# Optimization experiments

Hardware: AMD Instinct MI355X
Metric: run time of the kernel (lower is better)

Reference implementation:

```python
import jax, jax.numpy as jnp
import numpy as np

N = 100_000   # nodes
E = 1_600_000 # directed edges
G = 2048      # graphs in batch
NF = 78       # input node features
DIM = 32      # GIN hidden dim
L = 5         # num GIN layers
OUT = 128     # output_dim
BN_EPS = 1e-5


def setup_inputs() -> dict:
    key = jax.random.key(0)
    ks = jax.random.split(key, 8)
    s = 0.1
    return {
        "x": jax.random.normal(ks[0], (N, NF), jnp.float32),
        "edge_index": jax.random.randint(ks[1], (2, E), 0, N, jnp.int32),
        "batch": jnp.sort(jax.random.randint(ks[2], (N,), 0, G, jnp.int32)),
        "W1_0": (jax.random.normal(ks[3], (NF, DIM), jnp.float32) * s),
        "W1_rest": (jax.random.normal(ks[4], (L - 1, DIM, DIM), jnp.float32) * s),
        "b1": jnp.zeros((L, DIM), jnp.float32),
        "W2": (jax.random.normal(ks[5], (L, DIM, DIM), jnp.float32) * s),
        "b2": jnp.zeros((L, DIM), jnp.float32),
        "gamma": jnp.ones((L, DIM), jnp.float32),
        "beta": jnp.zeros((L, DIM), jnp.float32),
        "Wfc": (jax.random.normal(ks[6], (DIM, OUT), jnp.float32) * s),
        "bfc": jnp.zeros((OUT,), jnp.float32),
    }


def reference(x, edge_index, batch, W1_0, W1_rest, b1, W2, b2, gamma, beta, Wfc, bfc):
    src, dst = edge_index[0], edge_index[1]
    h = x
    for i in range(L):
        # GINConv (eps=0): h_i' = MLP(h_i + sum_{j->i} h_j)
        agg = jax.ops.segment_sum(h[src], dst, num_segments=N)  # [N, d]
        h = h + agg
        W1 = W1_0 if i == 0 else W1_rest[i - 1]
        h = jnp.maximum(h @ W1 + b1[i], 0.0) @ W2[i] + b2[i]
        # ReLU then BatchNorm1d (training mode: batch stats, biased var)
        h = jnp.maximum(h, 0.0)
        mu = h.mean(axis=0)
        var = h.var(axis=0)
        h = gamma[i] * (h - mu) * jax.lax.rsqrt(var + BN_EPS) + beta[i]
    pooled = jax.ops.segment_sum(h, batch, num_segments=G)  # global_add_pool [G, DIM]
    return jnp.maximum(pooled @ Wfc + bfc, 0.0)  # dropout is identity (eval)
```

## Files before the change

kernel.cpp:

```cpp
#include <hip/hip_runtime.h>
#include <hip/hip_fp16.h>

#define N_NODES 100000
#define N_EDGES 1600000
#define N_GRAPHS 2048
#define NFEAT 78
#define DIM 32
#define NLAYERS 5
#define OUTD 128
#define BN_EPS 1e-5f
#define NPB 32
#define NBUK 391
#define BNODES 256
#define STRIDE 4608
#define EPB 4096
#define NBLK ((N_EDGES + EPB - 1) / EPB)
#define NSLOTS2 ((N_NODES / NPB + 63) / 64)

__device__ __forceinline__ float2 up2(unsigned u) {
    __half2 h = *reinterpret_cast<__half2*>(&u);
    return __half22float2(h);
}
__device__ __forceinline__ unsigned pk2(float a, float b) {
    __half2 h = __floats2half2_rn(a, b);
    return *reinterpret_cast<unsigned*>(&h);
}

__global__ __launch_bounds__(256) void prep_kernel(
    const int* __restrict__ ei, int* __restrict__ bcnt, int* __restrict__ bdata,
    const float* __restrict__ x, const float* __restrict__ W1_0,
    unsigned short* __restrict__ y)
{
    __shared__ int cur[NBUK];
    __shared__ int gbl[NBUK];
    __shared__ float Wl[NFEAT * DIM];
    int tid = threadIdx.x;

    if (blockIdx.x < NBLK) {
        int base = blockIdx.x * EPB;
        for (int i = tid; i < NBUK; i += 256) cur[i] = 0;
        __syncthreads();

        int ew[16], eb[16];
        const int4* s4 = (const int4*)ei;
        const int4* d4 = (const int4*)(ei + N_EDGES);
#pragma unroll
        for (int c = 0; c < 4; ++c) {
            int eidx = base + c * 1024 + tid * 4;
            if (eidx < N_EDGES) {
                int4 sv = s4[eidx >> 2];
                int4 dv = d4[eidx >> 2];
                ew[c*4+0] = sv.x | ((dv.x & 255) << 17); eb[c*4+0] = dv.x >> 8;
                ew[c*4+1] = sv.y | ((dv.y & 255) << 17); eb[c*4+1] = dv.y >> 8;
                ew[c*4+2] = sv.z | ((dv.z & 255) << 17); eb[c*4+2] = dv.z >> 8;
                ew[c*4+3] = sv.w | ((dv.w & 255) << 17); eb[c*4+3] = dv.w >> 8;
            } else {
                eb[c*4+0] = eb[c*4+1] = eb[c*4+2] = eb[c*4+3] = -1;
                ew[c*4+0] = ew[c*4+1] = ew[c*4+2] = ew[c*4+3] = 0;
            }
        }
        int slot[16];
#pragma unroll
        for (int k = 0; k < 16; ++k)
            slot[k] = (eb[k] >= 0) ? atomicAdd(&cur[eb[k]], 1) : 0;
        __syncthreads();
        for (int b = tid; b < NBUK; b += 256) {
            int c = cur[b];
            gbl[b] = (c > 0) ? atomicAdd(&bcnt[b], c) : 0;
        }
        __syncthreads();
#pragma unroll
        for (int k = 0; k < 16; ++k) {
            int b = eb[k];
            if (b >= 0) {
                int pos = gbl[b] + slot[k];
                if (pos < STRIDE) bdata[b * STRIDE + pos] = ew[k];
            }
        }
    } else {
        for (int i = tid; i < NFEAT * DIM; i += 256) Wl[i] = W1_0[i];
        __syncthreads();
        int t = (blockIdx.x - NBLK) * 256 + tid;
        int row = t >> 3;
        int c0 = (t & 7) * 4;
        float a0 = 0.f, a1 = 0.f, a2 = 0.f, a3 = 0.f;
        const float* hr = x + (long)row * NFEAT;
        for (int k = 0; k < NFEAT; ++k) {
            float xv = hr[k];
            a0 = fmaf(xv, Wl[k * DIM + c0 + 0], a0);
            a1 = fmaf(xv, Wl[k * DIM + c0 + 1], a1);
            a2 = fmaf(xv, Wl[k * DIM + c0 + 2], a2);
            a3 = fmaf(xv, Wl[k * DIM + c0 + 3], a3);
        }
        ((uint2*)y)[(long)row * 8 + (t & 7)] = make_uint2(pk2(a0, a1), pk2(a2, a3));
    }
}

__global__ __launch_bounds__(512) void bscan_kernel(
    const int* __restrict__ bcnt, int* __restrict__ bbase)
{
    __shared__ int sd[512];
    int t = threadIdx.x;
    int v = (t < NBUK) ? min(bcnt[t], STRIDE) : 0;
    sd[t] = v; __syncthreads();
    for (int off = 1; off < 512; off <<= 1) {
        int a = (t >= off) ? sd[t - off] : 0;
        __syncthreads();
        sd[t] += a;
        __syncthreads();
    }
    if (t < NBUK) bbase[t + 1] = sd[t];
    if (t == 0) bbase[0] = 0;
}

__global__ __launch_bounds__(256) void cfill2_kernel(
    const int* __restrict__ bcnt, const int* __restrict__ bbase,
    const int* __restrict__ bdata, int* __restrict__ edge_src,
    int* __restrict__ offs)
{
    __shared__ int sorted[STRIDE];
    __shared__ int cnt[BNODES], off[BNODES], cur[BNODES];
    int b = blockIdx.x, tid = threadIdx.x;
    int n = min(bcnt[b], STRIDE);
    int gb = bbase[b];
    const int* slab = bdata + (long)b * STRIDE;

    if (tid < BNODES) cnt[tid] = 0;
    __syncthreads();
    for (int i = tid; i < n; i += 256)
        atomicAdd(&cnt[slab[i] >> 17], 1);
    __syncthreads();
    int t = tid;
    if (t < BNODES) off[t] = cnt[t];
    __syncthreads();
    for (int o = 1; o < BNODES; o <<= 1) {
        int a = (t >= o && t < BNODES) ? off[t - o] : 0;
        __syncthreads();
        if (t < BNODES) off[t] += a;
        __syncthreads();
    }
    if (t < BNODES) {
        int excl = off[t] - cnt[t];
        off[t] = excl;
        cur[t] = excl;
        int node = b * BNODES + t;
        if (node <= N_NODES) offs[node] = gb + excl;
    }
    __syncthreads();
    for (int i = tid; i < n; i += 256) {
        int w = slab[i];
        int pos = atomicAdd(&cur[w >> 17], 1);
        sorted[pos] = w & 0x1FFFF;
    }
    __syncthreads();
    for (int i = tid; i < n; i += 256)
        edge_src[gb + i] = sorted[i];
}

template<bool MM>
__global__ __launch_bounds__(256) void layer_kernel(
    const int* __restrict__ offs, const int* __restrict__ edge_src,
    const unsigned short* __restrict__ zin, const float* __restrict__ W1p,
    const float* __restrict__ cvec, const float* __restrict__ b1v,
    const float* __restrict__ W2, const float* __restrict__ b2v,
    unsigned short* __restrict__ zout, float* __restrict__ partial)
{
    __shared__ float W1l[DIM * DIM];
    __shared__ float W2l[DIM * DIM];
    __shared__ float zs[NPB][36];
    __shared__ float srow[NPB][36];
    __shared__ float b1l[DIM], b2l[DIM], cl[DIM];
    __shared__ float psum[DIM], psq[DIM];

    int tid = threadIdx.x;
    if (MM) for (int i = tid; i < DIM * DIM; i += 256) W1l[i] = W1p[i];
    for (int i = tid; i < DIM * DIM; i += 256) W2l[i] = W2[i];
    if (tid < DIM) {
        b1l[tid] = b1v[tid]; b2l[tid] = b2v[tid];
        cl[tid] = MM ? cvec[tid] : 0.f;
        psum[tid] = 0.f; psq[tid] = 0.f;
    }
    __syncthreads();

    int ln = tid >> 3, p = tid & 7;
    int c0 = p * 4;
    long node = (long)blockIdx.x * NPB + ln;
    int beg = offs[node], end = offs[node + 1];
    int deg = end - beg;
    const uint2* zb = (const uint2*)zin;

    uint2 sv = zb[node * 8 + p];
    float2 t01 = up2(sv.x), t23 = up2(sv.y);
    float a0 = t01.x, a1 = t01.y, a2 = t23.x, a3 = t23.y;
    int e = beg;
    for (; e + 8 <= end; e += 8) {
        uint2 v0 = zb[(long)edge_src[e + 0] * 8 + p];
        uint2 v1 = zb[(long)edge_src[e + 1] * 8 + p];
        uint2 v2 = zb[(long)edge_src[e + 2] * 8 + p];
        uint2 v3 = zb[(long)edge_src[e + 3] * 8 + p];
        uint2 v4 = zb[(long)edge_src[e + 4] * 8 + p];
        uint2 v5 = zb[(long)edge_src[e + 5] * 8 + p];
        uint2 v6 = zb[(long)edge_src[e + 6] * 8 + p];
        uint2 v7 = zb[(long)edge_src[e + 7] * 8 + p];
        float2 f;
        f = up2(v0.x); a0 += f.x; a1 += f.y;  f = up2(v0.y); a2 += f.x; a3 += f.y;
        f = up2(v1.x); a0 += f.x; a1 += f.y;  f = up2(v1.y); a2 += f.x; a3 += f.y;
        f = up2(v2.x); a0 += f.x; a1 += f.y;  f = up2(v2.y); a2 += f.x; a3 += f.y;
        f = up2(v3.x); a0 += f.x; a1 += f.y;  f = up2(v3.y); a2 += f.x; a3 += f.y;
        f = up2(v4.x); a0 += f.x; a1 += f.y;  f = up2(v4.y); a2 += f.x; a3 += f.y;
        f = up2(v5.x); a0 += f.x; a1 += f.y;  f = up2(v5.y); a2 += f.x; a3 += f.y;
        f = up2(v6.x); a0 += f.x; a1 += f.y;  f = up2(v6.y); a2 += f.x; a3 += f.y;
        f = up2(v7.x); a0 += f.x; a1 += f.y;  f = up2(v7.y); a2 += f.x; a3 += f.y;
    }
    for (; e < end; ++e) {
        uint2 v = zb[(long)edge_src[e] * 8 + p];
        float2 f;
        f = up2(v.x); a0 += f.x; a1 += f.y;
        f = up2(v.y); a2 += f.x; a3 += f.y;
    }
    *(float4*)&zs[ln][c0] = make_float4(a0, a1, a2, a3);

    float sv4[4];
    if (MM) {
        sv4[0] = sv4[1] = sv4[2] = sv4[3] = 0.f;
#pragma unroll
        for (int k = 0; k < DIM; ++k) {
            float zk = zs[ln][k];
            sv4[0] = fmaf(zk, W1l[k * DIM + c0 + 0], sv4[0]);
            sv4[1] = fmaf(zk, W1l[k * DIM + c0 + 1], sv4[1]);
            sv4[2] = fmaf(zk, W1l[k * DIM + c0 + 2], sv4[2]);
            sv4[3] = fmaf(zk, W1l[k * DIM + c0 + 3], sv4[3]);
        }
        float dp1 = (float)(deg + 1);
#pragma unroll
        for (int j = 0; j < 4; ++j)
            sv4[j] = fmaf(dp1, cl[c0 + j], sv4[j]) + b1l[c0 + j];
    } else {
        sv4[0] = a0 + b1l[c0 + 0]; sv4[1] = a1 + b1l[c0 + 1];
        sv4[2] = a2 + b1l[c0 + 2]; sv4[3] = a3 + b1l[c0 + 3];
    }
    float4 srw = make_float4(fmaxf(sv4[0], 0.f), fmaxf(sv4[1], 0.f),
                             fmaxf(sv4[2], 0.f), fmaxf(sv4[3], 0.f));
    *(float4*)&srow[ln][c0] = srw;

    float zv[4] = { b2l[c0 + 0], b2l[c0 + 1], b2l[c0 + 2], b2l[c0 + 3] };
#pragma unroll
    for (int k = 0; k < DIM; ++k) {
        float sk = srow[ln][k];
        zv[0] = fmaf(sk, W2l[k * DIM + c0 + 0], zv[0]);
        zv[1] = fmaf(sk, W2l[k * DIM + c0 + 1], zv[1]);
        zv[2] = fmaf(sk, W2l[k * DIM + c0 + 2], zv[2]);
        zv[3] = fmaf(sk, W2l[k * DIM + c0 + 3], zv[3]);
    }
#pragma unroll
    for (int j = 0; j < 4; ++j) zv[j] = fmaxf(zv[j], 0.f);
    ((uint2*)zout)[node * 8 + p] = make_uint2(pk2(zv[0], zv[1]), pk2(zv[2], zv[3]));

    float sq[4];
#pragma unroll
    for (int j = 0; j < 4; ++j) sq[j] = zv[j] * zv[j];
#pragma unroll
    for (int off = 8; off < 64; off <<= 1) {
#pragma unroll
        for (int j = 0; j < 4; ++j) {
            zv[j] += __shfl_xor(zv[j], off, 64);
            sq[j] += __shfl_xor(sq[j], off, 64);
        }
    }
    if ((tid & 63) < 8) {
#pragma unroll
        for (int j = 0; j < 4; ++j) {
            atomicAdd(&psum[c0 + j], zv[j]);
            atomicAdd(&psq[c0 + j], sq[j]);
        }
    }
    __syncthreads();
    if (tid < 2 * DIM) {
        float v = (tid < DIM) ? psum[tid] : psq[tid - DIM];
        atomicAdd(&partial[(long)(blockIdx.x >> 6) * 2 * DIM + tid], v);
    }
}

__global__ __launch_bounds__(256) void finalize_kernel(
    const float* __restrict__ partial,
    const float* __restrict__ gamma, const float* __restrict__ beta,
    float* __restrict__ ss, const float* W1next,
    float* __restrict__ W1p, float* __restrict__ cvec)
{
    __shared__ float red[256];
    __shared__ float sscl[DIM], sshl[DIM];
    int t = threadIdx.x;
    int c = t & 63;
    int chunk = t >> 6;
    float a = 0.f;
    for (int p = chunk; p < NSLOTS2; p += 4) a += partial[(long)p * 64 + c];
    red[t] = a; __syncthreads();
    if (t < 64) red[t] = red[t] + red[t + 64] + red[t + 128] + red[t + 192];
    __syncthreads();
    if (t < DIM) {
        const float invN = 1.0f / (float)N_NODES;
        float S = red[t], Q = red[t + DIM];
        float mu = S * invN;
        float var = Q * invN - mu * mu;
        float scale = gamma[t] * rsqrtf(var + BN_EPS);
        float shift = beta[t] - mu * scale;
        ss[t] = scale; ss[DIM + t] = shift;
        sscl[t] = scale; sshl[t] = shift;
    }
    __syncthreads();
    if (W1next) {
        for (int i = t; i < DIM * DIM; i += 256)
            W1p[i] = sscl[i >> 5] * W1next[i];
        if (t < DIM) {
            float cv = 0.f;
            for (int k = 0; k < DIM; ++k)
                cv += sshl[k] * W1next[k * DIM + t];
            cvec[t] = cv;
        }
    }
}

__global__ __launch_bounds__(256) void pool_kernel(
    const unsigned short* __restrict__ z, const int* __restrict__ batch,
    const float* __restrict__ ss, float* __restrict__ pooled)
{
    __shared__ float acc[32][32];
    __shared__ int slot[32];
    __shared__ int segg[32];
    __shared__ int nsegS;
    __shared__ float scl[DIM], shl[DIM];
    int tid = threadIdx.x;
    for (int i = tid; i < 1024; i += 256) ((float*)acc)[i] = 0.f;
    if (tid < DIM) { scl[tid] = ss[tid]; shl[tid] = ss[DIM + tid]; }
    int nodeBase = blockIdx.x * 32;
    if (tid < 32) {
        int nd = nodeBase + tid;
        int gv = batch[nd];
        int flag = (tid == 0) ? 1 : (gv != batch[nd - 1]);
        unsigned long long m = __ballot(flag);
        int s = __popcll(m & ((2ull << tid) - 1ull)) - 1;
        slot[tid] = s;
        if (flag) segg[s] = gv;
        if (tid == 0) nsegS = __popcll(m);
    }
    __syncthreads();

    int ln = tid >> 3;
    int p = tid & 7;
    long node = nodeBase + ln;
    uint2 u = ((const uint2*)z)[node * 8 + p];
    int c = p * 4;
    float2 f01 = up2(u.x), f23 = up2(u.y);
    float vx = fmaf(f01.x, scl[c+0], shl[c+0]);
    float vy = fmaf(f01.y, scl[c+1], shl[c+1]);
    float vz = fmaf(f23.x, scl[c+2], shl[c+2]);
    float vw = fmaf(f23.y, scl[c+3], shl[c+3]);
    int s = slot[ln];
    atomicAdd(&acc[s][c+0], vx);
    atomicAdd(&acc[s][c+1], vy);
    atomicAdd(&acc[s][c+2], vz);
    atomicAdd(&acc[s][c+3], vw);
    __syncthreads();

    int total = nsegS * 32;
    for (int i = tid; i < total; i += 256) {
        int r = i >> 5, dd = i & 31;
        float val = acc[r][dd];
        if (val != 0.f) atomicAdd(&pooled[(long)segg[r] * DIM + dd], val);
    }
}

__global__ __launch_bounds__(256) void fc_kernel(
    const float* __restrict__ pooled, const float* __restrict__ Wfc,
    const float* __restrict__ bfc, float* __restrict__ out)
{
    __shared__ float Wl[DIM * OUTD];
    for (int i = threadIdx.x; i < DIM * OUTD; i += 256) Wl[i] = Wfc[i];
    __syncthreads();
    int t = blockIdx.x * 256 + threadIdx.x;
    if (t >= N_GRAPHS * OUTD) return;
    int g = t >> 7;
    int o = t & (OUTD - 1);
    float acc = bfc[o];
    const float* pr = pooled + (long)g * DIM;
#pragma unroll
    for (int k = 0; k < DIM; ++k) acc += pr[k] * Wl[k * OUTD + o];
    out[t] = fmaxf(acc, 0.f);
}

extern "C" void kernel_launch(void* const* d_in, const int* in_sizes, int n_in,
                              void* d_out, int out_size, void* d_ws, size_t ws_size,
                              hipStream_t stream) {
    const float* x      = (const float*)d_in[0];
    const int*   ei     = (const int*)  d_in[1];
    const int*   batch  = (const int*)  d_in[2];
    const float* W1_0   = (const float*)d_in[3];
    const float* W1_rest= (const float*)d_in[4];
    const float* b1     = (const float*)d_in[5];
    const float* W2     = (const float*)d_in[6];
    const float* b2     = (const float*)d_in[7];
    const float* gamma  = (const float*)d_in[8];
    const float* beta   = (const float*)d_in[9];
    const float* Wfc    = (const float*)d_in[10];
    const float* bfc    = (const float*)d_in[11];
    float* out = (float*)d_out;

    int* wsi = (int*)d_ws;
    const size_t nf = (size_t)N_NODES * DIM;
    const size_t BD = (size_t)NBUK * STRIDE;
    int*   bdata  = wsi;
    unsigned short* zfpA = (unsigned short*)(wsi + BD);
    unsigned short* zfpB = zfpA + nf;
    int*   edge_src = (int*)(zfpB + nf);
    int*   offs   = edge_src + N_EDGES;
    int*   bcnt   = offs + (N_NODES + 1);
    int*   bbase  = bcnt + NBUK;
    float* pooled = (float*)(bbase + NBUK + 1);
    float* partial= pooled + (size_t)N_GRAPHS * DIM;
    float* ss     = partial + (size_t)NLAYERS * NSLOTS2 * 2 * DIM;
    float* W1p    = ss + NLAYERS * 2 * DIM;
    float* cvec   = W1p + NLAYERS * DIM * DIM;

    hipMemsetAsync(pooled, 0,
        ((size_t)N_GRAPHS * DIM + (size_t)NLAYERS * NSLOTS2 * 2 * DIM) *
        sizeof(float), stream);
    hipMemsetAsync(bcnt, 0, (size_t)NBUK * sizeof(int), stream);

    const int grpBlocks = (N_NODES * 8) / 256;

    prep_kernel<<<NBLK + grpBlocks, 256, 0, stream>>>(
        ei, bcnt, bdata, x, W1_0, zfpA);
    bscan_kernel<<<1, 512, 0, stream>>>(bcnt, bbase);
    cfill2_kernel<<<NBUK, 256, 0, stream>>>(bcnt, bbase, bdata, edge_src, offs);

    layer_kernel<false><<<N_NODES / NPB, 256, 0, stream>>>(
        offs, edge_src, zfpA, nullptr, nullptr,
        b1, W2, b2, zfpB, partial);
    finalize_kernel<<<1, 256, 0, stream>>>(
        partial, gamma, beta, ss,
        W1_rest, W1p + DIM * DIM, cvec + DIM);

    const unsigned short* zi = zfpB;
    unsigned short* zo = zfpA;
    for (int i = 1; i < NLAYERS; ++i) {
        layer_kernel<true><<<N_NODES / NPB, 256, 0, stream>>>(
            offs, edge_src, zi,
            W1p + (size_t)i * DIM * DIM, cvec + (size_t)i * DIM,
            b1 + i * DIM, W2 + (size_t)i * DIM * DIM, b2 + i * DIM,
            zo, partial + (size_t)i * NSLOTS2 * 2 * DIM);
        const float* W1next = (i + 1 < NLAYERS) ? (W1_rest + (size_t)i * DIM * DIM)
                                                : nullptr;
        finalize_kernel<<<1, 256, 0, stream>>>(
            partial + (size_t)i * NSLOTS2 * 2 * DIM,
            gamma + i * DIM, beta + i * DIM, ss + i * 2 * DIM,
            W1next, W1p + (size_t)(i + 1) * DIM * DIM,
            cvec + (size_t)(i + 1) * DIM);
        const unsigned short* tmp = zi; zi = zo; zo = (unsigned short*)tmp;
    }

    pool_kernel<<<N_NODES / 32, 256, 0, stream>>>(
        zi, batch, ss + (NLAYERS - 1) * 2 * DIM, pooled);
    fc_kernel<<<(N_GRAPHS * OUTD) / 256, 256, 0, stream>>>(pooled, Wfc, bfc, out);
}
```

Baseline: 301.4 us.

## Fuse BN finalize into layer and fc kernels; process two nodes per thread

Removes the single-block finalize kernel launches between layers. Each layer block now reduces the previous layer's partial BN statistics itself and folds scale and shift into W1. The final BN is applied algebraically in fc_kernel using per-graph node counts gathered by pool_kernel. Each layer block now handles 64 nodes, with each thread interleaving the gathers of two nodes to raise memory-level parallelism. The cost is redundant statistic reduction in every block and higher register use.

```diff
diff --git a/kernel.cpp b/kernel.cpp
--- a/kernel.cpp
+++ b/kernel.cpp
@@ -9,13 +9,13 @@
 #define NLAYERS 5
 #define OUTD 128
 #define BN_EPS 1e-5f
-#define NPB 32
 #define NBUK 391
 #define BNODES 256
 #define STRIDE 4608
 #define EPB 4096
 #define NBLK ((N_EDGES + EPB - 1) / EPB)
-#define NSLOTS2 ((N_NODES / NPB + 63) / 64)
+#define NLB ((N_NODES + 63) / 64)
+#define NSLOTS3 ((NLB + 63) / 64)
 
 __device__ __forceinline__ float2 up2(unsigned u) {
     __half2 h = *reinterpret_cast<__half2*>(&u);
@@ -160,117 +160,200 @@
 template<bool MM>
 __global__ __launch_bounds__(256) void layer_kernel(
     const int* __restrict__ offs, const int* __restrict__ edge_src,
-    const unsigned short* __restrict__ zin, const float* __restrict__ W1p,
-    const float* __restrict__ cvec, const float* __restrict__ b1v,
+    const unsigned short* __restrict__ zin,
+    const float* __restrict__ W1g,
+    const float* __restrict__ partial_prev,
+    const float* __restrict__ gprev, const float* __restrict__ bprev,
+    const float* __restrict__ b1v,
     const float* __restrict__ W2, const float* __restrict__ b2v,
     unsigned short* __restrict__ zout, float* __restrict__ partial)
 {
     __shared__ float W1l[DIM * DIM];
     __shared__ float W2l[DIM * DIM];
-    __shared__ float zs[NPB][36];
-    __shared__ float srow[NPB][36];
+    __shared__ float zs[64][36];
     __shared__ float b1l[DIM], b2l[DIM], cl[DIM];
+    __shared__ float sscl[DIM], sshl[DIM];
     __shared__ float psum[DIM], psq[DIM];
 
     int tid = threadIdx.x;
-    if (MM) for (int i = tid; i < DIM * DIM; i += 256) W1l[i] = W1p[i];
+    float* red = &zs[0][0];
+
     for (int i = tid; i < DIM * DIM; i += 256) W2l[i] = W2[i];
     if (tid < DIM) {
         b1l[tid] = b1v[tid]; b2l[tid] = b2v[tid];
-        cl[tid] = MM ? cvec[tid] : 0.f;
         psum[tid] = 0.f; psq[tid] = 0.f;
+    }
+    if (MM) {
+        int c = tid & 63, chunk = tid >> 6;
+        float a = 0.f;
+        for (int p = chunk; p < NSLOTS3; p += 4) a += partial_prev[p * 64 + c];
+        red[tid] = a;
+        __syncthreads();
+        if (tid < 64) red[tid] = red[tid] + red[tid+64] + red[tid+128] + red[tid+192];
+        __syncthreads();
+        if (tid < DIM) {
+            const float invN = 1.0f / (float)N_NODES;
+            float S = red[tid], Q = red[tid + DIM];
+            float mu = S * invN;
+            float var = Q * invN - mu * mu;
+            float sc = gprev[tid] * rsqrtf(var + BN_EPS);
+            sscl[tid] = sc;
+            sshl[tid] = bprev[tid] - mu * sc;
+        }
+        __syncthreads();
+        for (int i = tid; i < DIM * DIM; i += 256) W1l[i] = sscl[i >> 5] * W1g[i];
+        if (tid < DIM) {
+            float cv = 0.f;
+            for (int k = 0; k < DIM; ++k) cv = fmaf(sshl[k], W1g[k * DIM + tid], cv);
+            cl[tid] = cv;
+        }
     }
     __syncthreads();
 
     int ln = tid >> 3, p = tid & 7;
     int c0 = p * 4;
-    long node = (long)blockIdx.x * NPB + ln;
-    int beg = offs[node], end = offs[node + 1];
-    int deg = end - beg;
+    int nb = blockIdx.x * 64;
+    int nA = nb + ln;
+    int nB = nb + 32 + ln;
+    bool vB = nB < N_NODES;
+    int begA = offs[nA], endA = offs[nA + 1];
+    int begB = 0, endB = 0;
+    if (vB) { begB = offs[nB]; endB = offs[nB + 1]; }
+    int degA = endA - begA, degB = endB - begB;
     const uint2* zb = (const uint2*)zin;
 
-    uint2 sv = zb[node * 8 + p];
-    float2 t01 = up2(sv.x), t23 = up2(sv.y);
-    float a0 = t01.x, a1 = t01.y, a2 = t23.x, a3 = t23.y;
-    int e = beg;
-    for (; e + 8 <= end; e += 8) {
-        uint2 v0 = zb[(long)edge_src[e + 0] * 8 + p];
-        uint2 v1 = zb[(long)edge_src[e + 1] * 8 + p];
-        uint2 v2 = zb[(long)edge_src[e + 2] * 8 + p];
-        uint2 v3 = zb[(long)edge_src[e + 3] * 8 + p];
-        uint2 v4 = zb[(long)edge_src[e + 4] * 8 + p];
-        uint2 v5 = zb[(long)edge_src[e + 5] * 8 + p];
-        uint2 v6 = zb[(long)edge_src[e + 6] * 8 + p];
-        uint2 v7 = zb[(long)edge_src[e + 7] * 8 + p];
-        float2 f;
+    uint2 svA = zb[(long)nA * 8 + p];
+    float2 f;
+    f = up2(svA.x); float a0 = f.x, a1 = f.y;
+    f = up2(svA.y); float a2 = f.x, a3 = f.y;
+    float g0 = 0.f, g1 = 0.f, g2 = 0.f, g3 = 0.f;
+    if (vB) {
+        uint2 svB = zb[(long)nB * 8 + p];
+        f = up2(svB.x); g0 = f.x; g1 = f.y;
+        f = up2(svB.y); g2 = f.x; g3 = f.y;
+    }
+    int eA = begA, eB = begB;
+    for (; eA + 4 <= endA && eB + 4 <= endB; eA += 4, eB += 4) {
+        int sA0 = edge_src[eA+0], sA1 = edge_src[eA+1];
+        int sA2 = edge_src[eA+2], sA3 = edge_src[eA+3];
+        int sB0 = edge_src[eB+0], sB1 = edge_src[eB+1];
+        int sB2 = edge_src[eB+2], sB3 = edge_src[eB+3];
+        uint2 vA0 = zb[(long)sA0*8+p], vA1 = zb[(long)sA1*8+p];
+        uint2 vA2 = zb[(long)sA2*8+p], vA3 = zb[(long)sA3*8+p];
+        uint2 vB0 = zb[(long)sB0*8+p], vB1 = zb[(long)sB1*8+p];
+        uint2 vB2 = zb[(long)sB2*8+p], vB3 = zb[(long)sB3*8+p];
+        f = up2(vA0.x); a0 += f.x; a1 += f.y;  f = up2(vA0.y); a2 += f.x; a3 += f.y;
+        f = up2(vA1.x); a0 += f.x; a1 += f.y;  f = up2(vA1.y); a2 += f.x; a3 += f.y;
+        f = up2(vA2.x); a0 += f.x; a1 += f.y;  f = up2(vA2.y); a2 += f.x; a3 += f.y;
+        f = up2(vA3.x); a0 += f.x; a1 += f.y;  f = up2(vA3.y); a2 += f.x; a3 += f.y;
+        f = up2(vB0.x); g0 += f.x; g1 += f.y;  f = up2(vB0.y); g2 += f.x; g3 += f.y;
+        f = up2(vB1.x); g0 += f.x; g1 += f.y;  f = up2(vB1.y); g2 += f.x; g3 += f.y;
+        f = up2(vB2.x); g0 += f.x; g1 += f.y;  f = up2(vB2.y); g2 += f.x; g3 += f.y;
+        f = up2(vB3.x); g0 += f.x; g1 += f.y;  f = up2(vB3.y); g2 += f.x; g3 += f.y;
+    }
+    for (; eA + 4 <= endA; eA += 4) {
+        int s0 = edge_src[eA+0], s1 = edge_src[eA+1];
+        int s2 = edge_src[eA+2], s3 = edge_src[eA+3];
+        uint2 v0 = zb[(long)s0*8+p], v1 = zb[(long)s1*8+p];
+        uint2 v2 = zb[(long)s2*8+p], v3 = zb[(long)s3*8+p];
         f = up2(v0.x); a0 += f.x; a1 += f.y;  f = up2(v0.y); a2 += f.x; a3 += f.y;
         f = up2(v1.x); a0 += f.x; a1 += f.y;  f = up2(v1.y); a2 += f.x; a3 += f.y;
         f = up2(v2.x); a0 += f.x; a1 += f.y;  f = up2(v2.y); a2 += f.x; a3 += f.y;
         f = up2(v3.x); a0 += f.x; a1 += f.y;  f = up2(v3.y); a2 += f.x; a3 += f.y;
-        f = up2(v4.x); a0 += f.x; a1 += f.y;  f = up2(v4.y); a2 += f.x; a3 += f.y;
-        f = up2(v5.x); a0 += f.x; a1 += f.y;  f = up2(v5.y); a2 += f.x; a3 += f.y;
-        f = up2(v6.x); a0 += f.x; a1 += f.y;  f = up2(v6.y); a2 += f.x; a3 += f.y;
-        f = up2(v7.x); a0 += f.x; a1 += f.y;  f = up2(v7.y); a2 += f.x; a3 += f.y;
-    }
-    for (; e < end; ++e) {
-        uint2 v = zb[(long)edge_src[e] * 8 + p];
-        float2 f;
+    }
+    for (; eA < endA; ++eA) {
+        uint2 v = zb[(long)edge_src[eA]*8+p];
         f = up2(v.x); a0 += f.x; a1 += f.y;
         f = up2(v.y); a2 += f.x; a3 += f.y;
     }
-    *(float4*)&zs[ln][c0] = make_float4(a0, a1, a2, a3);
-
-    float sv4[4];
+    for (; eB + 4 <= endB; eB += 4) {
+        int s0 = edge_src[eB+0], s1 = edge_src[eB+1];
+        int s2 = edge_src[eB+2], s3 = edge_src[eB+3];
+        uint2 v0 = zb[(long)s0*8+p], v1 = zb[(long)s1*8+p];
+        uint2 v2 = zb[(long)s2*8+p], v3 = zb[(long)s3*8+p];
+        f = up2(v0.x); g0 += f.x; g1 += f.y;  f = up2(v0.y); g2 += f.x; g3 += f.y;
+        f = up2(v1.x); g0 += f.x; g1 += f.y;  f = up2(v1.y); g2 += f.x; g3 += f.y;
+        f = up2(v2.x); g0 += f.x; g1 += f.y;  f = up2(v2.y); g2 += f.x; g3 += f.y;
+        f = up2(v3.x); g0 += f.x; g1 += f.y;  f = up2(v3.y); g2 += f.x; g3 += f.y;
+    }
+    for (; eB < endB; ++eB) {
+        uint2 v = zb[(long)edge_src[eB]*8+p];
+        f = up2(v.x); g0 += f.x; g1 += f.y;
+        f = up2(v.y); g2 += f.x; g3 += f.y;
+    }
+    *(float4*)&zs[ln][c0]      = make_float4(a0, a1, a2, a3);
+    *(float4*)&zs[ln + 32][c0] = make_float4(g0, g1, g2, g3);
+
+    float tA[4], tB[4];
     if (MM) {
-        sv4[0] = sv4[1] = sv4[2] = sv4[3] = 0.f;
+        tA[0]=tA[1]=tA[2]=tA[3]=0.f; tB[0]=tB[1]=tB[2]=tB[3]=0.f;
 #pragma unroll
         for (int k = 0; k < DIM; ++k) {
+            float w0 = W1l[k * DIM + c0 + 0], w1 = W1l[k * DIM + c0 + 1];
+            float w2 = W1l[k * DIM + c0 + 2], w3 = W1l[k * DIM + c0 + 3];
             float zk = zs[ln][k];
-            sv4[0] = fmaf(zk, W1l[k * DIM + c0 + 0], sv4[0]);
-            sv4[1] = fmaf(zk, W1l[k * DIM + c0 + 1], sv4[1]);
-            sv4[2] = fmaf(zk, W1l[k * DIM + c0 + 2], sv4[2]);
-            sv4[3] = fmaf(zk, W1l[k * DIM + c0 + 3], sv4[3]);
-        }
-        float dp1 = (float)(deg + 1);
-#pragma unroll
-        for (int j = 0; j < 4; ++j)
-            sv4[j] = fmaf(dp1, cl[c0 + j], sv4[j]) + b1l[c0 + j];
+            tA[0] = fmaf(zk, w0, tA[0]); tA[1] = fmaf(zk, w1, tA[1]);
+            tA[2] = fmaf(zk, w2, tA[2]); tA[3] = fmaf(zk, w3, tA[3]);
+            float wk = zs[ln + 32][k];
+            tB[0] = fmaf(wk, w0, tB[0]); tB[1] = fmaf(wk, w1, tB[1]);
+            tB[2] = fmaf(wk, w2, tB[2]); tB[3] = fmaf(wk, w3, tB[3]);
+        }
+        float dA = (float)(degA + 1), dB = (float)(degB + 1);
+#pragma unroll
+        for (int j = 0; j < 4; ++j) {
+            tA[j] = fmaxf(fmaf(dA, cl[c0 + j], tA[j]) + b1l[c0 + j], 0.f);
+            tB[j] = fmaxf(fmaf(dB, cl[c0 + j], tB[j]) + b1l[c0 + j], 0.f);
+        }
     } else {
-        sv4[0] = a0 + b1l[c0 + 0]; sv4[1] = a1 + b1l[c0 + 1];
-        sv4[2] = a2 + b1l[c0 + 2]; sv4[3] = a3 + b1l[c0 + 3];
-    }
-    float4 srw = make_float4(fmaxf(sv4[0], 0.f), fmaxf(sv4[1], 0.f),
-                             fmaxf(sv4[2], 0.f), fmaxf(sv4[3], 0.f));
-    *(float4*)&srow[ln][c0] = srw;
-
-    float zv[4] = { b2l[c0 + 0], b2l[c0 + 1], b2l[c0 + 2], b2l[c0 + 3] };
+        tA[0] = fmaxf(a0 + b1l[c0 + 0], 0.f); tA[1] = fmaxf(a1 + b1l[c0 + 1], 0.f);
+        tA[2] = fmaxf(a2 + b1l[c0 + 2], 0.f); tA[3] = fmaxf(a3 + b1l[c0 + 3], 0.f);
+        tB[0] = fmaxf(g0 + b1l[c0 + 0], 0.f); tB[1] = fmaxf(g1 + b1l[c0 + 1], 0.f);
+        tB[2] = fmaxf(g2 + b1l[c0 + 2], 0.f); tB[3] = fmaxf(g3 + b1l[c0 + 3], 0.f);
+    }
+    *(float4*)&zs[ln][c0]      = make_float4(tA[0], tA[1], tA[2], tA[3]);
+    *(float4*)&zs[ln + 32][c0] = make_float4(tB[0], tB[1], tB[2], tB[3]);
+
+    float zA[4] = { b2l[c0+0], b2l[c0+1], b2l[c0+2], b2l[c0+3] };
+    float zB[4] = { b2l[c0+0], b2l[c0+1], b2l[c0+2], b2l[c0+3] };
 #pragma unroll
     for (int k = 0; k < DIM; ++k) {
-        float sk = srow[ln][k];
-        zv[0] = fmaf(sk, W2l[k * DIM + c0 + 0], zv[0]);
-        zv[1] = fmaf(sk, W2l[k * DIM + c0 + 1], zv[1]);
-        zv[2] = fmaf(sk, W2l[k * DIM + c0 + 2], zv[2]);
-        zv[3] = fmaf(sk, W2l[k * DIM + c0 + 3], zv[3]);
-    }
-#pragma unroll
-    for (int j = 0; j < 4; ++j) zv[j] = fmaxf(zv[j], 0.f);
-    ((uint2*)zout)[node * 8 + p] = make_uint2(pk2(zv[0], zv[1]), pk2(zv[2], zv[3]));
-
-    float sq[4];
-#pragma unroll
-    for (int j = 0; j < 4; ++j) sq[j] = zv[j] * zv[j];
+        float w0 = W2l[k * DIM + c0 + 0], w1 = W2l[k * DIM + c0 + 1];
+        float w2 = W2l[k * DIM + c0 + 2], w3 = W2l[k * DIM + c0 + 3];
+        float sk = zs[ln][k];
+        zA[0] = fmaf(sk, w0, zA[0]); zA[1] = fmaf(sk, w1, zA[1]);
+        zA[2] = fmaf(sk, w2, zA[2]); zA[3] = fmaf(sk, w3, zA[3]);
+        float rk = zs[ln + 32][k];
+        zB[0] = fmaf(rk, w0, zB[0]); zB[1] = fmaf(rk, w1, zB[1]);
+        zB[2] = fmaf(rk, w2, zB[2]); zB[3] = fmaf(rk, w3, zB[3]);
+    }
+#pragma unroll
+    for (int j = 0; j < 4; ++j) {
+        zA[j] = fmaxf(zA[j], 0.f);
+        zB[j] = fmaxf(zB[j], 0.f);
+    }
+    ((uint2*)zout)[(long)nA * 8 + p] = make_uint2(pk2(zA[0], zA[1]), pk2(zA[2], zA[3]));
+    if (vB)
+        ((uint2*)zout)[(long)nB * 8 + p] = make_uint2(pk2(zB[0], zB[1]), pk2(zB[2], zB[3]));
+    else { zB[0] = zB[1] = zB[2] = zB[3] = 0.f; }
+
+    float sv[4], sq[4];
+#pragma unroll
+    for (int j = 0; j < 4; ++j) {
+        sv[j] = zA[j] + zB[j];
+        sq[j] = zA[j]*zA[j] + zB[j]*zB[j];
+    }
 #pragma unroll
     for (int off = 8; off < 64; off <<= 1) {
 #pragma unroll
         for (int j = 0; j < 4; ++j) {
-            zv[j] += __shfl_xor(zv[j], off, 64);
+            sv[j] += __shfl_xor(sv[j], off, 64);
             sq[j] += __shfl_xor(sq[j], off, 64);
         }
     }
     if ((tid & 63) < 8) {
 #pragma unroll
         for (int j = 0; j < 4; ++j) {
-            atomicAdd(&psum[c0 + j], zv[j]);
+            atomicAdd(&psum[c0 + j], sv[j]);
             atomicAdd(&psq[c0 + j], sq[j]);
         }
     }
@@ -281,57 +364,18 @@
     }
 }
 
-__global__ __launch_bounds__(256) void finalize_kernel(
-    const float* __restrict__ partial,
-    const float* __restrict__ gamma, const float* __restrict__ beta,
-    float* __restrict__ ss, const float* W1next,
-    float* __restrict__ W1p, float* __restrict__ cvec)
-{
-    __shared__ float red[256];
-    __shared__ float sscl[DIM], sshl[DIM];
-    int t = threadIdx.x;
-    int c = t & 63;
-    int chunk = t >> 6;
-    float a = 0.f;
-    for (int p = chunk; p < NSLOTS2; p += 4) a += partial[(long)p * 64 + c];
-    red[t] = a; __syncthreads();
-    if (t < 64) red[t] = red[t] + red[t + 64] + red[t + 128] + red[t + 192];
-    __syncthreads();
-    if (t < DIM) {
-        const float invN = 1.0f / (float)N_NODES;
-        float S = red[t], Q = red[t + DIM];
-        float mu = S * invN;
-        float var = Q * invN - mu * mu;
-        float scale = gamma[t] * rsqrtf(var + BN_EPS);
-        float shift = beta[t] - mu * scale;
-        ss[t] = scale; ss[DIM + t] = shift;
-        sscl[t] = scale; sshl[t] = shift;
-    }
-    __syncthreads();
-    if (W1next) {
-        for (int i = t; i < DIM * DIM; i += 256)
-            W1p[i] = sscl[i >> 5] * W1next[i];
-        if (t < DIM) {
-            float cv = 0.f;
-            for (int k = 0; k < DIM; ++k)
-                cv += sshl[k] * W1next[k * DIM + t];
-            cvec[t] = cv;
-        }
-    }
-}
-
 __global__ __launch_bounds__(256) void pool_kernel(
     const unsigned short* __restrict__ z, const int* __restrict__ batch,
-    const float* __restrict__ ss, float* __restrict__ pooled)
+    float* __restrict__ praw, float* __restrict__ cntg)
 {
     __shared__ float acc[32][32];
+    __shared__ float cntL[32];
     __shared__ int slot[32];
     __shared__ int segg[32];
     __shared__ int nsegS;
-    __shared__ float scl[DIM], shl[DIM];
     int tid = threadIdx.x;
     for (int i = tid; i < 1024; i += 256) ((float*)acc)[i] = 0.f;
-    if (tid < DIM) { scl[tid] = ss[tid]; shl[tid] = ss[DIM + tid]; }
+    if (tid < 32) cntL[tid] = 0.f;
     int nodeBase = blockIdx.x * 32;
     if (tid < 32) {
         int nd = nodeBase + tid;
@@ -351,40 +395,68 @@
     uint2 u = ((const uint2*)z)[node * 8 + p];
     int c = p * 4;
     float2 f01 = up2(u.x), f23 = up2(u.y);
-    float vx = fmaf(f01.x, scl[c+0], shl[c+0]);
-    float vy = fmaf(f01.y, scl[c+1], shl[c+1]);
-    float vz = fmaf(f23.x, scl[c+2], shl[c+2]);
-    float vw = fmaf(f23.y, scl[c+3], shl[c+3]);
     int s = slot[ln];
-    atomicAdd(&acc[s][c+0], vx);
-    atomicAdd(&acc[s][c+1], vy);
-    atomicAdd(&acc[s][c+2], vz);
-    atomicAdd(&acc[s][c+3], vw);
+    atomicAdd(&acc[s][c+0], f01.x);
+    atomicAdd(&acc[s][c+1], f01.y);
+    atomicAdd(&acc[s][c+2], f23.x);
+    atomicAdd(&acc[s][c+3], f23.y);
+    if (p == 0) atomicAdd(&cntL[s], 1.f);
     __syncthreads();
 
     int total = nsegS * 32;
     for (int i = tid; i < total; i += 256) {
         int r = i >> 5, dd = i & 31;
         float val = acc[r][dd];
-        if (val != 0.f) atomicAdd(&pooled[(long)segg[r] * DIM + dd], val);
-    }
+        if (val != 0.f) atomicAdd(&praw[(long)segg[r] * DIM + dd], val);
+    }
+    if (tid < nsegS) atomicAdd(&cntg[segg[tid]], cntL[tid]);
 }
 
 __global__ __launch_bounds__(256) void fc_kernel(
-    const float* __restrict__ pooled, const float* __restrict__ Wfc,
-    const float* __restrict__ bfc, float* __restrict__ out)
+    const float* __restrict__ praw, const float* __restrict__ cntg,
+    const float* __restrict__ partial4,
+    const float* __restrict__ g4, const float* __restrict__ be4,
+    const float* __restrict__ Wfc, const float* __restrict__ bfc,
+    float* __restrict__ out)
 {
     __shared__ float Wl[DIM * OUTD];
-    for (int i = threadIdx.x; i < DIM * OUTD; i += 256) Wl[i] = Wfc[i];
-    __syncthreads();
-    int t = blockIdx.x * 256 + threadIdx.x;
-    if (t >= N_GRAPHS * OUTD) return;
+    __shared__ float red[256];
+    __shared__ float sscl[DIM], sshl[DIM], dvec[OUTD];
+    int tid = threadIdx.x;
+    for (int i = tid; i < DIM * OUTD; i += 256) Wl[i] = Wfc[i];
+    {
+        int c = tid & 63, chunk = tid >> 6;
+        float a = 0.f;
+        for (int p = chunk; p < NSLOTS3; p += 4) a += partial4[p * 64 + c];
+        red[tid] = a;
+    }
+    __syncthreads();
+    if (tid < 64) red[tid] = red[tid] + red[tid+64] + red[tid+128] + red[tid+192];
+    __syncthreads();
+    if (tid < DIM) {
+        const float invN = 1.0f / (float)N_NODES;
+        float S = red[tid], Q = red[tid + DIM];
+        float mu = S * invN;
+        float var = Q * invN - mu * mu;
+        float sc = g4[tid] * rsqrtf(var + BN_EPS);
+        sscl[tid] = sc;
+        sshl[tid] = be4[tid] - mu * sc;
+    }
+    __syncthreads();
+    if (tid < OUTD) {
+        float dv = 0.f;
+        for (int k = 0; k < DIM; ++k) dv = fmaf(sshl[k], Wl[k * OUTD + tid], dv);
+        dvec[tid] = dv;
+    }
+    __syncthreads();
+    int t = blockIdx.x * 256 + tid;
     int g = t >> 7;
     int o = t & (OUTD - 1);
-    float acc = bfc[o];
-    const float* pr = pooled + (long)g * DIM;
-#pragma unroll
-    for (int k = 0; k < DIM; ++k) acc += pr[k] * Wl[k * OUTD + o];
+    float acc = bfc[o] + cntg[g] * dvec[o];
+    const float* pr = praw + (long)g * DIM;
+#pragma unroll
+    for (int k = 0; k < DIM; ++k)
+        acc = fmaf(sscl[k] * pr[k], Wl[k * OUTD + o], acc);
     out[t] = fmaxf(acc, 0.f);
 }
 
@@ -408,6 +480,7 @@
     int* wsi = (int*)d_ws;
     const size_t nf = (size_t)N_NODES * DIM;
     const size_t BD = (size_t)NBUK * STRIDE;
+    const size_t PSTRIDE = (size_t)NSLOTS3 * 2 * DIM;
     int*   bdata  = wsi;
     unsigned short* zfpA = (unsigned short*)(wsi + BD);
     unsigned short* zfpB = zfpA + nf;
@@ -415,15 +488,13 @@
     int*   offs   = edge_src + N_EDGES;
     int*   bcnt   = offs + (N_NODES + 1);
     int*   bbase  = bcnt + NBUK;
-    float* pooled = (float*)(bbase + NBUK + 1);
-    float* partial= pooled + (size_t)N_GRAPHS * DIM;
-    float* ss     = partial + (size_t)NLAYERS * NSLOTS2 * 2 * DIM;
-    float* W1p    = ss + NLAYERS * 2 * DIM;
-    float* cvec   = W1p + NLAYERS * DIM * DIM;
-
-    hipMemsetAsync(pooled, 0,
-        ((size_t)N_GRAPHS * DIM + (size_t)NLAYERS * NSLOTS2 * 2 * DIM) *
-        sizeof(float), stream);
+    float* praw   = (float*)(bbase + NBUK + 1);
+    float* cntg   = praw + (size_t)N_GRAPHS * DIM;
+    float* partial= cntg + N_GRAPHS;
+
+    hipMemsetAsync(praw, 0,
+        ((size_t)N_GRAPHS * DIM + N_GRAPHS + NLAYERS * PSTRIDE) * sizeof(float),
+        stream);
     hipMemsetAsync(bcnt, 0, (size_t)NBUK * sizeof(int), stream);
 
     const int grpBlocks = (N_NODES * 8) / 256;
@@ -433,32 +504,26 @@
     bscan_kernel<<<1, 512, 0, stream>>>(bcnt, bbase);
     cfill2_kernel<<<NBUK, 256, 0, stream>>>(bcnt, bbase, bdata, edge_src, offs);
 
-    layer_kernel<false><<<N_NODES / NPB, 256, 0, stream>>>(
-        offs, edge_src, zfpA, nullptr, nullptr,
+    layer_kernel<false><<<NLB, 256, 0, stream>>>(
+        offs, edge_src, zfpA, nullptr, nullptr, nullptr, nullptr,
         b1, W2, b2, zfpB, partial);
-    finalize_kernel<<<1, 256, 0, stream>>>(
-        partial, gamma, beta, ss,
-        W1_rest, W1p + DIM * DIM, cvec + DIM);
 
     const unsigned short* zi = zfpB;
     unsigned short* zo = zfpA;
     for (int i = 1; i < NLAYERS; ++i) {
-        layer_kernel<true><<<N_NODES / NPB, 256, 0, stream>>>(
+        layer_kernel<true><<<NLB, 256, 0, stream>>>(
             offs, edge_src, zi,
-            W1p + (size_t)i * DIM * DIM, cvec + (size_t)i * DIM,
+            W1_rest + (size_t)(i - 1) * DIM * DIM,
+            partial + (size_t)(i - 1) * PSTRIDE,
+            gamma + (i - 1) * DIM, beta + (i - 1) * DIM,
             b1 + i * DIM, W2 + (size_t)i * DIM * DIM, b2 + i * DIM,
-            zo, partial + (size_t)i * NSLOTS2 * 2 * DIM);
-        const float* W1next = (i + 1 < NLAYERS) ? (W1_rest + (size_t)i * DIM * DIM)
-                                                : nullptr;
-        finalize_kernel<<<1, 256, 0, stream>>>(
-            partial + (size_t)i * NSLOTS2 * 2 * DIM,
-            gamma + i * DIM, beta + i * DIM, ss + i * 2 * DIM,
-            W1next, W1p + (size_t)(i + 1) * DIM * DIM,
-            cvec + (size_t)(i + 1) * DIM);
+            zo, partial + (size_t)i * PSTRIDE);
         const unsigned short* tmp = zi; zi = zo; zo = (unsigned short*)tmp;
     }
 
-    pool_kernel<<<N_NODES / 32, 256, 0, stream>>>(
-        zi, batch, ss + (NLAYERS - 1) * 2 * DIM, pooled);
-    fc_kernel<<<(N_GRAPHS * OUTD) / 256, 256, 0, stream>>>(pooled, Wfc, bfc, out);
-}
+    pool_kernel<<<N_NODES / 32, 256, 0, stream>>>(zi, batch, praw, cntg);
+    fc_kernel<<<(N_GRAPHS * OUTD) / 256, 256, 0, stream>>>(
+        praw, cntg, partial + (size_t)(NLAYERS - 1) * PSTRIDE,
+        gamma + (NLAYERS - 1) * DIM, beta + (NLAYERS - 1) * DIM,
+        Wfc, bfc, out);
+}
```

New measurement: 373.1 us. 1.24x slower.
